# Optimization experiments

Measured on AMD Instinct MI355X. Metric: run time of the kernel, lower is better.

## Reference

```python
import jax, jax.numpy as jnp
import numpy as np

N_NODES = 50000
N_EDGES = 800000
IN_FEATS = 128
OUT_FEATS = 128


def setup_inputs() -> dict:
    key = jax.random.key(0)
    k1, k2, k3, k4, k5 = jax.random.split(key, 5)
    # xavier_uniform for W
    limit = float(np.sqrt(6.0 / (IN_FEATS + OUT_FEATS)))
    W = jax.random.uniform(k2, (IN_FEATS, OUT_FEATS), jnp.float32, -limit, limit)
    return {
        "feat": jax.random.normal(k1, (N_NODES, IN_FEATS), jnp.float32),
        "W": W,
        "b": jnp.zeros((OUT_FEATS,), jnp.float32),
        "edge_w": jax.random.uniform(k3, (N_EDGES,), jnp.float32),
        "edge_src": jax.random.randint(k4, (N_EDGES,), 0, N_NODES),
        "edge_dst": jax.random.randint(k5, (N_EDGES,), 0, N_NODES),
    }


def reference(feat, W, b, edge_w, edge_src, edge_dst):
    N = feat.shape[0]
    ones = jnp.ones(edge_src.shape[0], feat.dtype)
    # norm == 'both': scale src features by out_degree^{-1/2}
    out_deg = jnp.clip(jax.ops.segment_sum(ones, edge_src, num_segments=N), 1.0)
    feat = feat * (out_deg ** -0.5)[:, None]  # [N, in]
    # in_feats (128) is NOT > out_feats (128): aggregate first, then matmul
    msgs = feat[edge_src] * edge_w[:, None]  # [E, in] (u_mul_e)
    agg = jax.ops.segment_sum(msgs, edge_dst, num_segments=N)  # [N, in] (sum)
    rst = agg @ W  # [N, out]
    # dst-side normalization: in_degree^{-1/2}
    in_deg = jnp.clip(jax.ops.segment_sum(ones, edge_dst, num_segments=N), 1.0)
    rst = rst * (in_deg ** -0.5)[:, None] + b
    return rst
```

## Files before the change

### kernel.cpp

```cpp
#include <hip/hip_runtime.h>
#include <math.h>

#define N_NODES 50000
#define N_EDGES 800000
#define F 128
#define CAP 64


__global__ __launch_bounds__(256) void place_kernel(
    const int* __restrict__ src, const int* __restrict__ dst,
    const float* __restrict__ edge_w,
    int* __restrict__ out_deg, int* __restrict__ cnt, int2* __restrict__ meta) {
    int e = blockIdx.x * blockDim.x + threadIdx.x;
    if (e >= N_EDGES) return;
    int s = src[e];
    int d = dst[e];
    atomicAdd(&out_deg[s], 1);
    int pos = atomicAdd(&cnt[d], 1);
    if (pos < CAP)
        meta[(size_t)d * CAP + pos] = make_int2(s, __float_as_int(edge_w[e]));
}

__global__ __launch_bounds__(256) void gather_kernel(
    const float* __restrict__ feat, const int* __restrict__ cnt,
    const int* __restrict__ out_deg, const int2* __restrict__ meta,
    float* __restrict__ agg) {
    int wid = (blockIdx.x * blockDim.x + threadIdx.x) >> 6;
    if (wid >= N_NODES) return;
    int lane = threadIdx.x & 63;
    int half = lane >> 5, l = lane & 31;
    int c = cnt[wid];
    if (c > CAP) c = CAP;
    const int2* m = meta + (size_t)wid * CAP;
    float4 acc = make_float4(0.f, 0.f, 0.f, 0.f);
    int j = half;
    for (; j + 2 < c; j += 4) {
        int2 m0 = m[j];
        int2 m1 = m[j + 2];
        float w0 = __int_as_float(m0.y) * rsqrtf(fmaxf((float)out_deg[m0.x], 1.0f));
        float w1 = __int_as_float(m1.y) * rsqrtf(fmaxf((float)out_deg[m1.x], 1.0f));
        float4 v0 = ((const float4*)(feat + (size_t)m0.x * F))[l];
        float4 v1 = ((const float4*)(feat + (size_t)m1.x * F))[l];
        acc.x += w0 * v0.x; acc.y += w0 * v0.y;
        acc.z += w0 * v0.z; acc.w += w0 * v0.w;
        acc.x += w1 * v1.x; acc.y += w1 * v1.y;
        acc.z += w1 * v1.z; acc.w += w1 * v1.w;
    }
    for (; j < c; j += 2) {
        int2 m0 = m[j];
        float w0 = __int_as_float(m0.y) * rsqrtf(fmaxf((float)out_deg[m0.x], 1.0f));
        float4 v0 = ((const float4*)(feat + (size_t)m0.x * F))[l];
        acc.x += w0 * v0.x; acc.y += w0 * v0.y;
        acc.z += w0 * v0.z; acc.w += w0 * v0.w;
    }
    acc.x += __shfl_xor(acc.x, 32, 64);
    acc.y += __shfl_xor(acc.y, 32, 64);
    acc.z += __shfl_xor(acc.z, 32, 64);
    acc.w += __shfl_xor(acc.w, 32, 64);
    if (half == 0)
        ((float4*)(agg + (size_t)wid * F))[l] = acc;
}

__global__ __launch_bounds__(256) void gemm_inplace(
    const float* __restrict__ W, const float* __restrict__ bias,
    const int* __restrict__ cnt, float* __restrict__ io) {
    __shared__ float As[64][36];
    __shared__ float Ws[32][128];

    int tid = threadIdx.x;
    int row0 = blockIdx.x * 64;
    int tx = tid & 15, ty = tid >> 4;

    float acc[4][8] = {{0.f}};
    for (int kt = 0; kt < 4; ++kt) {
        __syncthreads();
#pragma unroll
        for (int p = 0; p < 2; ++p) {
            int q = tid + p * 256;
            int r = q >> 3, c4 = q & 7;
            int gr = row0 + r;
            float4 v = make_float4(0.f, 0.f, 0.f, 0.f);
            if (gr < N_NODES)
                v = ((const float4*)(io + (size_t)gr * F + kt * 32))[c4];
            *(float4*)&As[r][c4 * 4] = v;
        }
#pragma unroll
        for (int p = 0; p < 4; ++p) {
            int q = tid + p * 256;
            int r = q >> 5, c4 = q & 31;
            *(float4*)&Ws[r][c4 * 4] = ((const float4*)(W + (size_t)(kt * 32 + r) * F))[c4];
        }
        __syncthreads();
#pragma unroll
        for (int k = 0; k < 32; ++k) {
            float a[4];
#pragma unroll
            for (int i = 0; i < 4; ++i) a[i] = As[ty * 4 + i][k];
            float4 b0 = *(float4*)&Ws[k][tx * 4];
            float4 b1 = *(float4*)&Ws[k][64 + tx * 4];
#pragma unroll
            for (int i = 0; i < 4; ++i) {
                acc[i][0] += a[i] * b0.x;
                acc[i][1] += a[i] * b0.y;
                acc[i][2] += a[i] * b0.z;
                acc[i][3] += a[i] * b0.w;
                acc[i][4] += a[i] * b1.x;
                acc[i][5] += a[i] * b1.y;
                acc[i][6] += a[i] * b1.z;
                acc[i][7] += a[i] * b1.w;
            }
        }
    }

#pragma unroll
    for (int i = 0; i < 4; ++i) {
        int gr = row0 + ty * 4 + i;
        if (gr >= N_NODES) continue;
        float sc = rsqrtf(fmaxf((float)cnt[gr], 1.0f));
        float4 o0, o1;
        o0.x = acc[i][0] * sc + bias[tx * 4 + 0];
        o0.y = acc[i][1] * sc + bias[tx * 4 + 1];
        o0.z = acc[i][2] * sc + bias[tx * 4 + 2];
        o0.w = acc[i][3] * sc + bias[tx * 4 + 3];
        o1.x = acc[i][4] * sc + bias[64 + tx * 4 + 0];
        o1.y = acc[i][5] * sc + bias[64 + tx * 4 + 1];
        o1.z = acc[i][6] * sc + bias[64 + tx * 4 + 2];
        o1.w = acc[i][7] * sc + bias[64 + tx * 4 + 3];
        ((float4*)(io + (size_t)gr * F))[tx] = o0;
        ((float4*)(io + (size_t)gr * F))[16 + tx] = o1;
    }
}

extern "C" void kernel_launch(void* const* d_in, const int* in_sizes, int n_in,
                              void* d_out, int out_size, void* d_ws, size_t ws_size,
                              hipStream_t stream) {
    const float* feat   = (const float*)d_in[0];
    const float* W      = (const float*)d_in[1];
    const float* bias   = (const float*)d_in[2];
    const float* edge_w = (const float*)d_in[3];
    const int* edge_src = (const int*)d_in[4];
    const int* edge_dst = (const int*)d_in[5];
    float* out = (float*)d_out;

    int2* meta   = (int2*)d_ws;
    int* cnt     = (int*)((char*)d_ws + (size_t)N_NODES * CAP * sizeof(int2));
    int* out_deg = cnt + N_NODES;

    hipMemsetAsync(cnt, 0, (size_t)2 * N_NODES * sizeof(int), stream);

    place_kernel<<<(N_EDGES + 255) / 256, 256, 0, stream>>>(
        edge_src, edge_dst, edge_w, out_deg, cnt, meta);

    gather_kernel<<<(N_NODES * 64 + 255) / 256, 256, 0, stream>>>(
        feat, cnt, out_deg, meta, out);

    gemm_inplace<<<(N_NODES + 63) / 64, 256, 0, stream>>>(
        W, bias, cnt, out);
}
```

Measured before the change: 249.7 us.

## Compute out-degree via per-block shared-memory histograms with packed 16-bit counters

Removes the global atomic out-degree increment from the edge placement kernel. A separate histogram kernel builds per-block partial counts in shared memory, packing two 16-bit counters per word and making two passes over node halves. A reduce kernel then sums the partials and writes a precomputed rsqrt table that the gather reads. This trades scattered global atomics for two extra launches, shared-memory atomics and a partial buffer that reuses the meta workspace. Only 64 blocks run the histogram, so its parallelism is limited.

```diff
diff --git a/kernel.cpp b/kernel.cpp
--- a/kernel.cpp
+++ b/kernel.cpp
@@ -5,17 +5,61 @@
 #define N_EDGES 800000
 #define F 128
 #define CAP 64
-
+#define NB 64
+#define EPB 12500
+#define HALF 25000
+#define SLOTS 12500
+
+
+__global__ __launch_bounds__(256) void hist_kernel(
+    const int* __restrict__ src, unsigned* __restrict__ partial) {
+    __shared__ unsigned h[SLOTS];
+    int b = blockIdx.x, tid = threadIdx.x;
+    int e0 = b * EPB;
+    int e1 = e0 + EPB;
+    if (e1 > N_EDGES) e1 = N_EDGES;
+    for (int h2 = 0; h2 < 2; ++h2) {
+        for (int j = tid; j < SLOTS; j += 256) h[j] = 0;
+        __syncthreads();
+        int base = h2 * HALF;
+        for (int e = e0 + tid; e < e1; e += 256) {
+            int s = src[e];
+            unsigned us = (unsigned)(s - base);
+            if (us < HALF)
+                atomicAdd(&h[us >> 1], 1u << ((s & 1) * 16));
+        }
+        __syncthreads();
+        unsigned* po = partial + ((size_t)h2 * NB + b) * SLOTS;
+        for (int j = tid; j < SLOTS; j += 256) po[j] = h[j];
+        __syncthreads();
+    }
+}
+
+__global__ __launch_bounds__(256) void reduce_kernel(
+    const unsigned* __restrict__ partial, float* __restrict__ inv_od) {
+    int t = blockIdx.x * blockDim.x + threadIdx.x;
+    if (t >= 2 * SLOTS) return;
+    int h2 = t / SLOTS, j = t - h2 * SLOTS;
+    const unsigned* p = partial + (size_t)h2 * NB * SLOTS + j;
+    unsigned lo = 0, hi = 0;
+    for (int b = 0; b < NB; ++b) {
+        unsigned v = p[(size_t)b * SLOTS];
+        lo += v & 0xFFFFu;
+        hi += v >> 16;
+    }
+    int n0 = h2 * HALF + 2 * j;
+    inv_od[n0] = rsqrtf(fmaxf((float)lo, 1.0f));
+    inv_od[n0 + 1] = rsqrtf(fmaxf((float)hi, 1.0f));
+}
 
 __global__ __launch_bounds__(256) void place_kernel(
     const int* __restrict__ src, const int* __restrict__ dst,
     const float* __restrict__ edge_w,
-    int* __restrict__ out_deg, int* __restrict__ cnt, int2* __restrict__ meta) {
+    int* __restrict__ cnt, int2* __restrict__ meta) {
     int e = blockIdx.x * blockDim.x + threadIdx.x;
     if (e >= N_EDGES) return;
     int s = src[e];
     int d = dst[e];
-    atomicAdd(&out_deg[s], 1);
     int pos = atomicAdd(&cnt[d], 1);
     if (pos < CAP)
         meta[(size_t)d * CAP + pos] = make_int2(s, __float_as_int(edge_w[e]));
@@ -23,7 +67,7 @@
 
 __global__ __launch_bounds__(256) void gather_kernel(
     const float* __restrict__ feat, const int* __restrict__ cnt,
-    const int* __restrict__ out_deg, const int2* __restrict__ meta,
+    const float* __restrict__ inv_od, const int2* __restrict__ meta,
     float* __restrict__ agg) {
     int wid = (blockIdx.x * blockDim.x + threadIdx.x) >> 6;
     if (wid >= N_NODES) return;
@@ -37,8 +81,8 @@
     for (; j + 2 < c; j += 4) {
         int2 m0 = m[j];
         int2 m1 = m[j + 2];
-        float w0 = __int_as_float(m0.y) * rsqrtf(fmaxf((float)out_deg[m0.x], 1.0f));
-        float w1 = __int_as_float(m1.y) * rsqrtf(fmaxf((float)out_deg[m1.x], 1.0f));
+        float w0 = __int_as_float(m0.y) * inv_od[m0.x];
+        float w1 = __int_as_float(m1.y) * inv_od[m1.x];
         float4 v0 = ((const float4*)(feat + (size_t)m0.x * F))[l];
         float4 v1 = ((const float4*)(feat + (size_t)m1.x * F))[l];
         acc.x += w0 * v0.x; acc.y += w0 * v0.y;
@@ -48,7 +92,7 @@
     }
     for (; j < c; j += 2) {
         int2 m0 = m[j];
-        float w0 = __int_as_float(m0.y) * rsqrtf(fmaxf((float)out_deg[m0.x], 1.0f));
+        float w0 = __int_as_float(m0.y) * inv_od[m0.x];
         float4 v0 = ((const float4*)(feat + (size_t)m0.x * F))[l];
         acc.x += w0 * v0.x; acc.y += w0 * v0.y;
         acc.z += w0 * v0.z; acc.w += w0 * v0.w;
@@ -142,17 +186,21 @@
     const int* edge_dst = (const int*)d_in[5];
     float* out = (float*)d_out;
 
-    int2* meta   = (int2*)d_ws;
-    int* cnt     = (int*)((char*)d_ws + (size_t)N_NODES * CAP * sizeof(int2));
-    int* out_deg = cnt + N_NODES;
-
-    hipMemsetAsync(cnt, 0, (size_t)2 * N_NODES * sizeof(int), stream);
+    int2* meta     = (int2*)d_ws;
+    int* cnt       = (int*)((char*)d_ws + (size_t)N_NODES * CAP * sizeof(int2));
+    float* inv_od  = (float*)(cnt + N_NODES);
+    unsigned* part = (unsigned*)d_ws;
+
+    hipMemsetAsync(cnt, 0, (size_t)N_NODES * sizeof(int), stream);
+
+    hist_kernel<<<NB, 256, 0, stream>>>(edge_src, part);
+    reduce_kernel<<<(2 * SLOTS + 255) / 256, 256, 0, stream>>>(part, inv_od);
 
     place_kernel<<<(N_EDGES + 255) / 256, 256, 0, stream>>>(
-        edge_src, edge_dst, edge_w, out_deg, cnt, meta);
+        edge_src, edge_dst, edge_w, cnt, meta);
 
     gather_kernel<<<(N_NODES * 64 + 255) / 256, 256, 0, stream>>>(
-        feat, cnt, out_deg, meta, out);
+        feat, cnt, inv_od, meta, out);
 
     gemm_inplace<<<(N_NODES + 63) / 64, 256, 0, stream>>>(
         W, bias, cnt, out);
```

New measurement: 249.0 us. About the same (-0.3%).
